# Kernel tuning notes

Measured on AMD Instinct MI355X. Metric: run time of the kernel, lower is better.

## Reference

```python
import jax, jax.numpy as jnp
import numpy as np

B, IN, H = 4096, 1024, 1024
G = 5  # i, f, o, c_hat, s gates

def setup_inputs() -> dict:
    key = jax.random.key(0)
    ks = jax.random.split(key, 24)
    s_in = 1.0 / np.sqrt(IN)
    s_h = 1.0 / np.sqrt(H)
    s_cat = 1.0 / np.sqrt(IN + H)
    inp = {
        'x': jax.random.normal(ks[0], (B, IN), jnp.float32),
        'h_prev': jax.random.normal(ks[1], (B, H), jnp.float32),
        'c_prev': jax.random.normal(ks[2], (B, H), jnp.float32),
        'ssg_state': jax.random.normal(ks[3], (B, H), jnp.float32),
        # stacked gate weights, torch Linear convention y = x @ W.T + b
        'Wx': jax.random.uniform(ks[4], (G, H, IN), jnp.float32, -s_in, s_in),
        'bWx': jax.random.uniform(ks[5], (G, H), jnp.float32, -s_in, s_in),
        'Ux': jax.random.uniform(ks[6], (G, H, H), jnp.float32, -s_h, s_h),
        'bUx': jax.random.uniform(ks[7], (G, H), jnp.float32, -s_h, s_h),
        # alpha MLP: Linear(IN+H -> H), ReLU, Linear(H -> 1), Sigmoid
        'a1_w': jax.random.uniform(ks[8], (H, IN + H), jnp.float32, -s_cat, s_cat),
        'a1_b': jax.random.uniform(ks[9], (H,), jnp.float32, -s_cat, s_cat),
        'a2_w': jax.random.uniform(ks[10], (1, H), jnp.float32, -s_h, s_h),
        'a2_b': jax.random.uniform(ks[11], (1,), jnp.float32, -s_h, s_h),
        'r1_w': jax.random.uniform(ks[12], (H, H), jnp.float32, -s_h, s_h),
        'r1_b': jax.random.uniform(ks[13], (H,), jnp.float32, -s_h, s_h),
        'r2_w': jax.random.uniform(ks[14], (H, H), jnp.float32, -s_h, s_h),
        'r2_b': jax.random.uniform(ks[15], (H,), jnp.float32, -s_h, s_h),
        'r3_w': jax.random.uniform(ks[16], (H, H), jnp.float32, -s_h, s_h),
        'r3_b': jax.random.uniform(ks[17], (H,), jnp.float32, -s_h, s_h),
        'ssg_w': jax.random.uniform(ks[18], (H, H), jnp.float32, -s_h, s_h),
        'ssg_b': jax.random.uniform(ks[19], (H,), jnp.float32, -s_h, s_h),
    }
    return inp


def reference(x, h_prev, c_prev, ssg_state, Wx, bWx, Ux, bUx,
              a1_w, a1_b, a2_w, a2_b, r1_w, r1_b, r2_w, r2_b, r3_w, r3_b,
              ssg_w, ssg_b):
    # all 5 gate pre-activations in two batched GEMMs: [G, B, H]
    g = (jnp.einsum('bi,ghi->gbh', x, Wx) + bWx[:, None, :]
         + jnp.einsum('bh,gkh->gbk', h_prev, Ux) + bUx[:, None, :])
    i_t = jax.nn.sigmoid(g[0])
    f_t = jax.nn.sigmoid(g[1])
    o_t = jax.nn.sigmoid(g[2])
    c_hat_t = jnp.tanh(g[3])
    s_t = jax.nn.sigmoid(g[4])  # computed as in original (unused when ssg_state given)

    combined = jnp.concatenate([x, h_prev], axis=-1)  # [B, IN+H]
    a_hidden = jax.nn.relu(combined @ a1_w.T + a1_b)
    alpha_t = jax.nn.sigmoid(a_hidden @ a2_w.T + a2_b)  # [B, 1]

    ssg_new = (ssg_state + h_prev) @ ssg_w.T + ssg_b  # ssg_state is not None branch

    c_t = f_t * c_prev + i_t * c_hat_t * s_t * alpha_t * ssg_new

    r = jax.nn.relu(h_prev @ r1_w.T + r1_b)
    r = jax.nn.relu(r @ r2_w.T + r2_b)
    residual = r @ r3_w.T + r3_b

    c_t = c_t + residual
    h_t = o_t * jnp.tanh(c_t)
    return (h_t, c_t, ssg_new)
```

## Files before the change

kernel.cpp:

```cpp
#include <hip/hip_runtime.h>
#include <hip/hip_bf16.h>

#define B_DIM 4096
#define H_DIM 1024
#define K1    2048
#define N1    6144

typedef __attribute__((ext_vector_type(8))) short bf16x8;
typedef __attribute__((ext_vector_type(4))) float f32x4;

__device__ __forceinline__ unsigned short f2bf(float f) {
  unsigned int x = __float_as_uint(f);
  x += 0x7fffu + ((x >> 16) & 1u);
  return (unsigned short)(x >> 16);
}
__device__ __forceinline__ float bf2f(unsigned short u) {
  return __uint_as_float(((unsigned int)u) << 16);
}
__device__ __forceinline__ float fast_sigmoid(float x) {
  return __builtin_amdgcn_rcpf(1.0f + __expf(-x));
}
__device__ __forceinline__ float fast_tanh(float x) {
  return 1.0f - 2.0f * __builtin_amdgcn_rcpf(1.0f + __expf(2.0f * x));
}
__device__ __forceinline__ void gload_lds16(const void* g, void* l) {
  __builtin_amdgcn_global_load_lds(
      (const __attribute__((address_space(1))) void*)g,
      (__attribute__((address_space(3))) void*)l, 16, 0, 0);
}

__device__ __forceinline__ int swz1k(int x) {
  return x ^ (((x >> 9) & 1) << 5);
}

__global__ __launch_bounds__(256) void prep_kernel(
    const float* __restrict__ x, const float* __restrict__ h,
    const float* __restrict__ ssg_state,
    const float* __restrict__ Wx, const float* __restrict__ Ux,
    const float* __restrict__ a1_w,
    const float* __restrict__ ssg_w, const float* __restrict__ r1_w,
    const float* __restrict__ r2_w, const float* __restrict__ r3_w,
    unsigned short* __restrict__ combined,
    unsigned short* __restrict__ ssg_in,
    unsigned short* __restrict__ W1,
    unsigned short* __restrict__ W2,
    unsigned short* __restrict__ W3,
    unsigned short* __restrict__ W4)
{
  const size_t NV0 = (size_t)B_DIM * K1 / 4;
  const size_t NV1 = (size_t)B_DIM * H_DIM / 4;
  const size_t NV3 = (size_t)N1 * K1 / 4;
  const size_t NV4 = (size_t)2048 * H_DIM / 4;
  const size_t NV5 = (size_t)H_DIM * H_DIM / 4;
  const size_t total = NV0 + NV1 + NV3 + NV4 + NV5 + NV5;
  const size_t stride = (size_t)gridDim.x * blockDim.x;

  for (size_t v = (size_t)blockIdx.x * blockDim.x + threadIdx.x; v < total; v += stride) {
    size_t idx = v;
    const float* src;
    unsigned short* dst;
    if (idx < NV0) {
      size_t e = idx * 4, b = e >> 11, k = e & 2047;
      src = (k < 1024) ? &x[(b << 10) + k] : &h[(b << 10) + (k - 1024)];
      dst = &combined[e];
    } else if ((idx -= NV0) < NV1) {
      size_t e = idx * 4;
      float4 a = *(const float4*)&ssg_state[e];
      float4 c = *(const float4*)&h[e];
      ushort4 o;
      o.x = f2bf(a.x + c.x); o.y = f2bf(a.y + c.y);
      o.z = f2bf(a.z + c.z); o.w = f2bf(a.w + c.w);
      *(ushort4*)&ssg_in[e] = o;
      continue;
    } else if ((idx -= NV1) < NV3) {
      size_t e = idx * 4, n = e >> 11, k = e & 2047;
      if (n < 5120) src = (k < 1024) ? &Wx[(n << 10) + k] : &Ux[(n << 10) + (k - 1024)];
      else          src = &a1_w[((n - 5120) << 11) + k];
      dst = &W1[e];
    } else if ((idx -= NV3) < NV4) {
      size_t e = idx * 4, n = e >> 10, k = e & 1023;
      src = (n < 1024) ? &ssg_w[(n << 10) + k] : &r1_w[((n - 1024) << 10) + k];
      dst = &W2[e];
    } else if ((idx -= NV4) < NV5) {
      size_t e = idx * 4; src = &r2_w[e]; dst = &W3[e];
    } else {
      idx -= NV5;
      size_t e = idx * 4; src = &r3_w[e]; dst = &W4[e];
    }
    float4 a = *(const float4*)src;
    ushort4 o;
    o.x = f2bf(a.x); o.y = f2bf(a.y); o.z = f2bf(a.z); o.w = f2bf(a.w);
    *(ushort4*)dst = o;
  }
}

template <int NT, int MODE>
__device__ __forceinline__ void gemm_body(
    unsigned short* lds, const int bid,
    const unsigned short* __restrict__ A0,
    const unsigned short* __restrict__ A1,
    const unsigned short* __restrict__ W,
    const float* __restrict__ b0, const float* __restrict__ b1,
    const float* __restrict__ b2,
    void* __restrict__ out0, void* __restrict__ out1)
{
  constexpr int KDIM = NT * 64;
  constexpr int NTN  = (MODE == 0) ? 48 : (MODE == 1 ? 16 : 8);
  constexpr int NWG  = 32 * NTN;

  const int tid  = threadIdx.x;
  const int wave = tid >> 6;
  const int lane = tid & 63;
  const int wm = wave >> 1;
  const int wn = wave & 1;

  const int swz = (bid & 7) * (NWG / 8) + (bid >> 3);
  const int tm = swz / NTN, tn = swz % NTN;
  const int tmB = tm * 128, tnB = tn * 128;

  const unsigned short* Abase = A0;
  int lda = (MODE == 0) ? K1 : 1024;
  if (MODE == 1 && tn >= 8) { Abase = A1; lda = 2048; }

  const int sidx = swz1k(lane * 16);
  const int r_l  = sidx >> 6;
  const int kel  = (sidx & 63) >> 1;
  const unsigned short* pA[2][2];
  const unsigned short* pB[2][2];
#pragma unroll
  for (int rg = 0; rg < 2; ++rg)
#pragma unroll
    for (int j = 0; j < 2; ++j) {
      const int rr = wave * 32 + rg * 16 + r_l;
      const int kk0 = j * 32 + kel;
      pA[rg][j] = Abase + (size_t)(tmB + rr) * lda + kk0;
      pB[rg][j] = W + (size_t)(tnB + rr) * KDIM + kk0;
    }

#define STAGE_A(tt) do { const int p_ = (tt) & 1;                                \
    _Pragma("unroll")                                                            \
    for (int rg = 0; rg < 2; ++rg)                                               \
      _Pragma("unroll")                                                          \
      for (int j = 0; j < 2; ++j)                                                \
        gload_lds16(pA[rg][j] + (size_t)(tt) * 64,                               \
                    &lds[p_ * 16384 + ((wave * 2 + rg) * 2 + j) * 512]);         \
  } while (0)
#define STAGE_B(tt) do { const int p_ = (tt) & 1;                                \
    _Pragma("unroll")                                                            \
    for (int rg = 0; rg < 2; ++rg)                                               \
      _Pragma("unroll")                                                          \
      for (int j = 0; j < 2; ++j)                                                \
        gload_lds16(pB[rg][j] + (size_t)(tt) * 64,                               \
                    &lds[p_ * 16384 + 8192 + ((wave * 2 + rg) * 2 + j) * 512]);  \
  } while (0)

  const int loc = swz1k((lane & 15) * 64 + (lane >> 4) * 16);

  f32x4 acc[4][4];
#pragma unroll
  for (int m = 0; m < 4; ++m)
#pragma unroll
    for (int n = 0; n < 4; ++n) acc[m][n] = (f32x4){0.f, 0.f, 0.f, 0.f};

  STAGE_A(0); STAGE_B(0);

#define MFMA16(aV, bV) do {                                                      \
    _Pragma("unroll")                                                            \
    for (int n = 0; n < 4; ++n) {                                                \
      _Pragma("unroll")                                                          \
      for (int m = 0; m < 4; ++m)                                                \
        acc[m][n] = __builtin_amdgcn_mfma_f32_16x16x32_bf16(                     \
            aV[m], bV[n], acc[m][n], 0, 0, 0);                                   \
    } } while (0)

  const char* lchar = (const char*)lds;
  for (int t = 0; t < NT; ++t) {
    asm volatile("s_waitcnt vmcnt(0)" ::: "memory");
    __builtin_amdgcn_s_barrier();

    const char* base = lchar + (t & 1) * 32768;
    const char* bA = base + wm * 8192 + loc;
    const char* bB = base + 16384 + wn * 8192 + loc;

    bf16x8 a0[4], a1[4], b0v[4], b1v[4];
#pragma unroll
    for (int n = 0; n < 4; ++n) b0v[n] = *(const bf16x8*)(bB + (2 * n + 0) * 1024);
#pragma unroll
    for (int m = 0; m < 4; ++m) a0[m] = *(const bf16x8*)(bA + (2 * m + 0) * 1024);
    if (t + 1 < NT) STAGE_A(t + 1);
#pragma unroll
    for (int n = 0; n < 4; ++n) b1v[n] = *(const bf16x8*)(bB + (2 * n + 1) * 1024);
#pragma unroll
    for (int m = 0; m < 4; ++m) a1[m] = *(const bf16x8*)(bA + (2 * m + 1) * 1024);
    if (t + 1 < NT) STAGE_B(t + 1);

    __builtin_amdgcn_s_setprio(1);
    MFMA16(a0, b0v);
    __builtin_amdgcn_s_setprio(0);
    __builtin_amdgcn_s_setprio(1);
    MFMA16(a1, b1v);
    __builtin_amdgcn_s_setprio(0);
  }
#undef MFMA16
#undef STAGE_A
#undef STAGE_B

  const int l15 = lane & 15, lq4 = (lane >> 4) << 2;
  const int rowg0 = tmB + wm * 64;

  if ((MODE == 1 && tn < 8) || MODE == 3) {
    const int col0 = tn * 128 + wn * 64;
#pragma unroll
    for (int fn = 0; fn < 4; ++fn) {
      const int col = col0 + fn * 16 + l15;
      const float bias = b0[col];
#pragma unroll
      for (int fm = 0; fm < 4; ++fm) {
        f32x4 v = acc[fm][fn];
#pragma unroll
        for (int j = 0; j < 4; ++j) {
          const int r = rowg0 + fm * 16 + lq4 + j;
          ((float*)out0)[(size_t)r * 1024 + col] = v[j] + bias;
        }
      }
    }
    return;
  }

  unsigned short* slab = &lds[wave * 1024];
  const int lr8 = lane >> 3, lc8 = lane & 7;
  bool isgate = false;
  int g = 0, colg0;
  unsigned short* outbase;
  if (MODE == 0) {
    isgate = (tn < 40);
    g = tn >> 3;
    colg0 = (isgate ? (tn & 7) : (tn - 40)) * 128 + wn * 64;
    outbase = isgate ? ((unsigned short*)out0 + (size_t)g * ((size_t)B_DIM * 1024))
                     : (unsigned short*)out1;
  } else if (MODE == 1) {
    colg0 = (tn - 8) * 128 + wn * 64;
    outbase = (unsigned short*)out1;
  } else {
    colg0 = tn * 128 + wn * 64;
    outbase = (unsigned short*)out1;
  }
  float biasv[4];
#pragma unroll
  for (int fn = 0; fn < 4; ++fn) {
    const int c = colg0 + fn * 16 + l15;
    if (MODE == 0) biasv[fn] = isgate ? (b0[g * 1024 + c] + b1[g * 1024 + c]) : b2[c];
    else           biasv[fn] = b1[c];
  }
  __builtin_amdgcn_s_barrier();
#pragma unroll
  for (int fm = 0; fm < 4; ++fm) {
#pragma unroll
    for (int fn = 0; fn < 4; ++fn) {
      f32x4 v = acc[fm][fn];
#pragma unroll
      for (int j = 0; j < 4; ++j) {
        const int row = lq4 + j;
        const float xv = v[j] + biasv[fn];
        float res;
        if (MODE == 0 && isgate) res = (g == 3) ? fast_tanh(xv) : fast_sigmoid(xv);
        else                     res = fmaxf(xv, 0.f);
        const int colb = ((fn * 16 + l15) * 2) ^ (((row >> 2) & 3) << 5);
        slab[(row * 128 + colb) >> 1] = f2bf(res);
      }
    }
    asm volatile("s_waitcnt lgkmcnt(0)" ::: "memory");
    __builtin_amdgcn_sched_barrier(0);
#pragma unroll
    for (int rd = 0; rd < 2; ++rd) {
      const int row = rd * 8 + lr8;
      const int cb = (lc8 * 16) ^ (((row >> 2) & 3) << 5);
      bf16x8 pk = *(const bf16x8*)((const char*)slab + row * 128 + cb);
      const size_t r = (size_t)(rowg0 + fm * 16 + row);
      *(bf16x8*)&outbase[r * 1024 + colg0 + lc8 * 8] = pk;
    }
    asm volatile("s_waitcnt lgkmcnt(0)" ::: "memory");
    __builtin_amdgcn_sched_barrier(0);
  }
}

__global__ __launch_bounds__(256, 2) void gemm_big(
    const unsigned short* __restrict__ combined,
    const unsigned short* __restrict__ ssg_in,
    const unsigned short* __restrict__ W1,
    const unsigned short* __restrict__ W2,
    const float* __restrict__ bWx, const float* __restrict__ bUx,
    const float* __restrict__ a1_b,
    const float* __restrict__ ssg_b, const float* __restrict__ r1_b,
    unsigned short* __restrict__ gates,
    unsigned short* __restrict__ a_hidden,
    float* __restrict__ ssg_out,
    unsigned short* __restrict__ r1)
{
  __shared__ unsigned short lds[32768];
  const int bid = blockIdx.x;
  if (bid < 1536) {
    gemm_body<32, 0>(lds, bid, combined, nullptr, W1,
                     bWx, bUx, a1_b, gates, a_hidden);
  } else {
    gemm_body<16, 1>(lds, bid - 1536, ssg_in, combined + 1024, W2,
                     ssg_b, r1_b, nullptr, ssg_out, r1);
  }
}

template <int MODE>
__global__ __launch_bounds__(256, 2) void gemm_small(
    const unsigned short* __restrict__ A,
    const unsigned short* __restrict__ W,
    const float* __restrict__ bias,
    void* __restrict__ out)
{
  __shared__ unsigned short lds[32768];
  if (MODE == 2) gemm_body<16, 2>(lds, blockIdx.x, A, nullptr, W,
                                  nullptr, bias, nullptr, nullptr, out);
  else           gemm_body<16, 3>(lds, blockIdx.x, A, nullptr, W,
                                  bias, nullptr, nullptr, out, nullptr);
}

__global__ __launch_bounds__(256) void final_fused(
    const unsigned short* __restrict__ gates,
    const float* __restrict__ c_prev,
    const unsigned short* __restrict__ a_hidden,
    const float* __restrict__ a2_w, const float* __restrict__ a2_b,
    const float* __restrict__ residual,
    const float* __restrict__ ssg_new,
    float* __restrict__ h_out, float* __restrict__ c_out)
{
  __shared__ float red[5];
  const int r = blockIdx.x;
  const int tid = threadIdx.x;
  const size_t BH = (size_t)B_DIM * H_DIM;

  {
    ushort4 u = *(const ushort4*)&a_hidden[(size_t)r * 1024 + tid * 4];
    float4 w = *(const float4*)&a2_w[tid * 4];
    float s = bf2f(u.x) * w.x + bf2f(u.y) * w.y + bf2f(u.z) * w.z + bf2f(u.w) * w.w;
#pragma unroll
    for (int off = 32; off; off >>= 1) s += __shfl_xor(s, off);
    if ((tid & 63) == 0) red[tid >> 6] = s;
  }
  __syncthreads();
  if (tid == 0)
    red[4] = fast_sigmoid(red[0] + red[1] + red[2] + red[3] + a2_b[0]);
  __syncthreads();
  const float al = red[4];

  const size_t e = (size_t)r * 1024 + tid * 4;
  ushort4 iu = *(const ushort4*)&gates[e];
  ushort4 fu = *(const ushort4*)&gates[BH + e];
  ushort4 ou = *(const ushort4*)&gates[2 * BH + e];
  ushort4 cu = *(const ushort4*)&gates[3 * BH + e];
  ushort4 su = *(const ushort4*)&gates[4 * BH + e];
  float4 cp = *(const float4*)&c_prev[e];
  float4 rs = *(const float4*)&residual[e];
  float4 sg = *(const float4*)&ssg_new[e];
  float4 ho, co;
  co.x = bf2f(fu.x) * cp.x + bf2f(iu.x) * bf2f(cu.x) * bf2f(su.x) * al * sg.x + rs.x;
  co.y = bf2f(fu.y) * cp.y + bf2f(iu.y) * bf2f(cu.y) * bf2f(su.y) * al * sg.y + rs.y;
  co.z = bf2f(fu.z) * cp.z + bf2f(iu.z) * bf2f(cu.z) * bf2f(su.z) * al * sg.z + rs.z;
  co.w = bf2f(fu.w) * cp.w + bf2f(iu.w) * bf2f(cu.w) * bf2f(su.w) * al * sg.w + rs.w;
  ho.x = bf2f(ou.x) * fast_tanh(co.x);
  ho.y = bf2f(ou.y) * fast_tanh(co.y);
  ho.z = bf2f(ou.z) * fast_tanh(co.z);
  ho.w = bf2f(ou.w) * fast_tanh(co.w);
  *(float4*)&h_out[e] = ho;
  *(float4*)&c_out[e] = co;
}

extern "C" void kernel_launch(void* const* d_in, const int* in_sizes, int n_in,
                              void* d_out, int out_size, void* d_ws, size_t ws_size,
                              hipStream_t stream)
{
  (void)in_sizes; (void)n_in; (void)out_size; (void)ws_size;
  const float* x         = (const float*)d_in[0];
  const float* h_prev    = (const float*)d_in[1];
  const float* c_prev    = (const float*)d_in[2];
  const float* ssg_state = (const float*)d_in[3];
  const float* Wx        = (const float*)d_in[4];
  const float* bWx       = (const float*)d_in[5];
  const float* Ux        = (const float*)d_in[6];
  const float* bUx       = (const float*)d_in[7];
  const float* a1_w      = (const float*)d_in[8];
  const float* a1_b      = (const float*)d_in[9];
  const float* a2_w      = (const float*)d_in[10];
  const float* a2_b      = (const float*)d_in[11];
  const float* r1_w      = (const float*)d_in[12];
  const float* r1_b      = (const float*)d_in[13];
  const float* r2_w      = (const float*)d_in[14];
  const float* r2_b      = (const float*)d_in[15];
  const float* r3_w      = (const float*)d_in[16];
  const float* r3_b      = (const float*)d_in[17];
  const float* ssg_w     = (const float*)d_in[18];
  const float* ssg_b     = (const float*)d_in[19];

  char* ws = (char*)d_ws;
  unsigned short* combined = (unsigned short*)(ws);
  unsigned short* ssg_in   = (unsigned short*)(ws + 16777216);
  unsigned short* W1       = (unsigned short*)(ws + 33554432);
  unsigned short* W2       = (unsigned short*)(ws + 58720256);
  unsigned short* W3       = (unsigned short*)(ws + 62914560);
  unsigned short* W4       = (unsigned short*)(ws + 65011712);
  unsigned short* gates    = (unsigned short*)(ws + 67108864);
  unsigned short* a_hidden = (unsigned short*)(ws + 109051904);
  unsigned short* r1       = (unsigned short*)(ws + 117456896);
  unsigned short* r2       = (unsigned short*)(ws + 125845504);
  float*          residual = (float*)(ws + 134234112);

  float* h_out   = (float*)d_out;
  float* c_out   = h_out + (size_t)B_DIM * H_DIM;
  float* ssg_out = c_out + (size_t)B_DIM * H_DIM;

  prep_kernel<<<4096, 256, 0, stream>>>(x, h_prev, ssg_state, Wx, Ux, a1_w,
                                        ssg_w, r1_w, r2_w, r3_w,
                                        combined, ssg_in, W1, W2, W3, W4);

  gemm_big<<<2048, 256, 0, stream>>>(
      combined, ssg_in, W1, W2, bWx, bUx, a1_b, ssg_b, r1_b,
      gates, a_hidden, ssg_out, r1);

  gemm_small<2><<<256, 256, 0, stream>>>(r1, W3, r2_b, r2);

  gemm_small<3><<<256, 256, 0, stream>>>(r2, W4, r3_b, residual);

  final_fused<<<B_DIM, 256, 0, stream>>>(
      gates, c_prev, a_hidden, a2_w, a2_b, residual, ssg_out, h_out, c_out);
}
```

Before: 224.0 us.

## Use 128x192 output tiles for the big gate GEMM to raise reuse

```diff
diff --git a/kernel.cpp b/kernel.cpp
--- a/kernel.cpp
+++ b/kernel.cpp
@@ -94,6 +94,169 @@
   }
 }
 
+__device__ __forceinline__ void body192(
+    unsigned short* lds, const int bid,
+    const unsigned short* __restrict__ A,
+    const unsigned short* __restrict__ W,
+    const float* __restrict__ bWx, const float* __restrict__ bUx,
+    const float* __restrict__ a1_b,
+    unsigned short* __restrict__ gates,
+    unsigned short* __restrict__ a_hidden)
+{
+  constexpr int NT  = 32;
+  constexpr int NTN = 32;
+  constexpr int NWG = 32 * NTN;
+
+  const int tid  = threadIdx.x;
+  const int wave = tid >> 6;
+  const int lane = tid & 63;
+  const int wm = wave >> 1;
+  const int wn = wave & 1;
+
+  const int swz = (bid & 7) * (NWG / 8) + (bid >> 3);
+  const int tm = swz / NTN, tn = swz % NTN;
+  const int tmB = tm * 128, tnB = tn * 192;
+
+  const int sidx = swz1k(lane * 16);
+  const int r_l  = sidx >> 6;
+  const int kel  = (sidx & 63) >> 1;
+  const unsigned short* pA[2][2];
+  const unsigned short* pB[3][2];
+#pragma unroll
+  for (int rg = 0; rg < 2; ++rg)
+#pragma unroll
+    for (int j = 0; j < 2; ++j)
+      pA[rg][j] = A + (size_t)(tmB + (wave * 2 + rg) * 16 + r_l) * K1 + j * 32 + kel;
+#pragma unroll
+  for (int rg = 0; rg < 3; ++rg)
+#pragma unroll
+    for (int j = 0; j < 2; ++j)
+      pB[rg][j] = W + (size_t)(tnB + (wave * 3 + rg) * 16 + r_l) * K1 + j * 32 + kel;
+
+#define STAGE_A(tt) do { const int p_ = (tt) & 1;                                \
+    _Pragma("unroll")                                                            \
+    for (int rg = 0; rg < 2; ++rg)                                               \
+      _Pragma("unroll")                                                          \
+      for (int j = 0; j < 2; ++j)                                                \
+        gload_lds16(pA[rg][j] + (size_t)(tt) * 64,                               \
+                    &lds[p_ * 20480 + ((wave * 2 + rg) * 2 + j) * 512]);         \
+  } while (0)
+#define STAGE_B(tt) do { const int p_ = (tt) & 1;                                \
+    _Pragma("unroll")                                                            \
+    for (int rg = 0; rg < 3; ++rg)                                               \
+      _Pragma("unroll")                                                          \
+      for (int j = 0; j < 2; ++j)                                                \
+        gload_lds16(pB[rg][j] + (size_t)(tt) * 64,                               \
+                    &lds[p_ * 20480 + 8192 + ((wave * 3 + rg) * 2 + j) * 512]);  \
+  } while (0)
+
+  const int loc = swz1k((lane & 15) * 64 + (lane >> 4) * 16);
+
+  f32x4 acc[4][6];
+#pragma unroll
+  for (int m = 0; m < 4; ++m)
+#pragma unroll
+    for (int n = 0; n < 6; ++n) acc[m][n] = (f32x4){0.f, 0.f, 0.f, 0.f};
+
+  STAGE_A(0); STAGE_B(0);
+
+#define MFMA24(aV, bV) do {                                                      \
+    _Pragma("unroll")                                                            \
+    for (int n = 0; n < 6; ++n) {                                                \
+      _Pragma("unroll")                                                          \
+      for (int m = 0; m < 4; ++m)                                                \
+        acc[m][n] = __builtin_amdgcn_mfma_f32_16x16x32_bf16(                     \
+            aV[m], bV[n], acc[m][n], 0, 0, 0);                                   \
+    } } while (0)
+
+  const char* lchar = (const char*)lds;
+  for (int t = 0; t < NT; ++t) {
+    asm volatile("s_waitcnt vmcnt(0)" ::: "memory");
+    __builtin_amdgcn_s_barrier();
+
+    const char* base = lchar + (t & 1) * 40960;
+    const char* bA = base + wm * 8192 + loc;
+    const char* bB = base + 16384 + wn * 12288 + loc;
+
+    bf16x8 a0[4], a1[4], b0[6], b1[6];
+#pragma unroll
+    for (int n = 0; n < 6; ++n) b0[n] = *(const bf16x8*)(bB + (2 * n + 0) * 1024);
+#pragma unroll
+    for (int m = 0; m < 4; ++m) a0[m] = *(const bf16x8*)(bA + (2 * m + 0) * 1024);
+    if (t + 1 < NT) STAGE_A(t + 1);
+#pragma unroll
+    for (int n = 0; n < 6; ++n) b1[n] = *(const bf16x8*)(bB + (2 * n + 1) * 1024);
+#pragma unroll
+    for (int m = 0; m < 4; ++m) a1[m] = *(const bf16x8*)(bA + (2 * m + 1) * 1024);
+    if (t + 1 < NT) STAGE_B(t + 1);
+
+    __builtin_amdgcn_s_setprio(1);
+    MFMA24(a0, b0);
+    __builtin_amdgcn_s_setprio(0);
+    __builtin_amdgcn_s_setprio(1);
+    MFMA24(a1, b1);
+    __builtin_amdgcn_s_setprio(0);
+  }
+#undef MFMA24
+#undef STAGE_A
+#undef STAGE_B
+
+  unsigned short* slab = &lds[wave * 1536];
+  const int l15 = lane & 15, lq4 = (lane >> 4) << 2;
+  const int colg0 = tnB + wn * 96;
+  const int rowg0 = tmB + wm * 64;
+  const size_t BH = (size_t)B_DIM * H_DIM;
+
+  float biasv[6];
+  int amode[6];
+#pragma unroll
+  for (int fn = 0; fn < 6; ++fn) {
+    const int c = colg0 + fn * 16 + l15;
+    if (c < 5120) {
+      biasv[fn] = bWx[c] + bUx[c];
+      amode[fn] = ((c >> 10) == 3) ? 1 : 0;
+    } else {
+      biasv[fn] = a1_b[c - 5120];
+      amode[fn] = 2;
+    }
+  }
+  __builtin_amdgcn_s_barrier();
+#pragma unroll
+  for (int fm = 0; fm < 4; ++fm) {
+#pragma unroll
+    for (int fn = 0; fn < 6; ++fn) {
+      f32x4 v = acc[fm][fn];
+#pragma unroll
+      for (int j = 0; j < 4; ++j) {
+        const int row = lq4 + j;
+        const float xv = v[j] + biasv[fn];
+        const float res = (amode[fn] == 1) ? fast_tanh(xv)
+                         : (amode[fn] == 0) ? fast_sigmoid(xv)
+                         : fmaxf(xv, 0.f);
+        const int byte = (row * 192 + (fn * 16 + l15) * 2) ^ (((row >> 2) & 1) << 5);
+        slab[byte >> 1] = f2bf(res);
+      }
+    }
+    asm volatile("s_waitcnt lgkmcnt(0)" ::: "memory");
+    __builtin_amdgcn_sched_barrier(0);
+#pragma unroll
+    for (int p = 0; p < 3; ++p) {
+      const int id = p * 64 + lane;
+      const int row = id / 12, cc = id - row * 12;
+      const int byte = (row * 192 + cc * 16) ^ (((row >> 2) & 1) << 5);
+      bf16x8 pk = *(const bf16x8*)((const char*)slab + byte);
+      const int col = colg0 + cc * 8;
+      const size_t r = (size_t)(rowg0 + fm * 16 + row);
+      unsigned short* dst;
+      if (col < 5120) dst = gates + (size_t)(col >> 10) * BH + r * 1024 + (col & 1023);
+      else            dst = a_hidden + r * 1024 + (col - 5120);
+      *(bf16x8*)dst = pk;
+    }
+    asm volatile("s_waitcnt lgkmcnt(0)" ::: "memory");
+    __builtin_amdgcn_sched_barrier(0);
+  }
+}
+
 template <int NT, int MODE>
 __device__ __forceinline__ void gemm_body(
     unsigned short* lds, const int bid,
@@ -101,11 +264,10 @@
     const unsigned short* __restrict__ A1,
     const unsigned short* __restrict__ W,
     const float* __restrict__ b0, const float* __restrict__ b1,
-    const float* __restrict__ b2,
     void* __restrict__ out0, void* __restrict__ out1)
 {
   constexpr int KDIM = NT * 64;
-  constexpr int NTN  = (MODE == 0) ? 48 : (MODE == 1 ? 16 : 8);
+  constexpr int NTN  = (MODE == 1) ? 16 : 8;
   constexpr int NWG  = 32 * NTN;
 
   const int tid  = threadIdx.x;
@@ -119,7 +281,7 @@
   const int tmB = tm * 128, tnB = tn * 128;
 
   const unsigned short* Abase = A0;
-  int lda = (MODE == 0) ? K1 : 1024;
+  int lda = 1024;
   if (MODE == 1 && tn >= 8) { Abase = A1; lda = 2048; }
 
   const int sidx = swz1k(lane * 16);
@@ -229,29 +391,13 @@
 
   unsigned short* slab = &lds[wave * 1024];
   const int lr8 = lane >> 3, lc8 = lane & 7;
-  bool isgate = false;
-  int g = 0, colg0;
-  unsigned short* outbase;
-  if (MODE == 0) {
-    isgate = (tn < 40);
-    g = tn >> 3;
-    colg0 = (isgate ? (tn & 7) : (tn - 40)) * 128 + wn * 64;
-    outbase = isgate ? ((unsigned short*)out0 + (size_t)g * ((size_t)B_DIM * 1024))
-                     : (unsigned short*)out1;
-  } else if (MODE == 1) {
-    colg0 = (tn - 8) * 128 + wn * 64;
-    outbase = (unsigned short*)out1;
-  } else {
-    colg0 = tn * 128 + wn * 64;
-    outbase = (unsigned short*)out1;
-  }
+  int colg0;
+  unsigned short* outbase = (unsigned short*)out1;
+  if (MODE == 1) colg0 = (tn - 8) * 128 + wn * 64;
+  else           colg0 = tn * 128 + wn * 64;
   float biasv[4];
 #pragma unroll
-  for (int fn = 0; fn < 4; ++fn) {
-    const int c = colg0 + fn * 16 + l15;
-    if (MODE == 0) biasv[fn] = isgate ? (b0[g * 1024 + c] + b1[g * 1024 + c]) : b2[c];
-    else           biasv[fn] = b1[c];
-  }
+  for (int fn = 0; fn < 4; ++fn) biasv[fn] = b1[colg0 + fn * 16 + l15];
   __builtin_amdgcn_s_barrier();
 #pragma unroll
   for (int fm = 0; fm < 4; ++fm) {
@@ -261,10 +407,7 @@
 #pragma unroll
       for (int j = 0; j < 4; ++j) {
         const int row = lq4 + j;
-        const float xv = v[j] + biasv[fn];
-        float res;
-        if (MODE == 0 && isgate) res = (g == 3) ? fast_tanh(xv) : fast_sigmoid(xv);
-        else                     res = fmaxf(xv, 0.f);
+        const float res = fmaxf(v[j] + biasv[fn], 0.f);
         const int colb = ((fn * 16 + l15) * 2) ^ (((row >> 2) & 3) << 5);
         slab[(row * 128 + colb) >> 1] = f2bf(res);
       }
@@ -297,14 +440,13 @@
     float* __restrict__ ssg_out,
     unsigned short* __restrict__ r1)
 {
-  __shared__ unsigned short lds[32768];
+  __shared__ unsigned short lds[40960];
   const int bid = blockIdx.x;
-  if (bid < 1536) {
-    gemm_body<32, 0>(lds, bid, combined, nullptr, W1,
-                     bWx, bUx, a1_b, gates, a_hidden);
+  if (bid < 1024) {
+    body192(lds, bid, combined, W1, bWx, bUx, a1_b, gates, a_hidden);
   } else {
-    gemm_body<16, 1>(lds, bid - 1536, ssg_in, combined + 1024, W2,
-                     ssg_b, r1_b, nullptr, ssg_out, r1);
+    gemm_body<16, 1>(lds, bid - 1024, ssg_in, combined + 1024, W2,
+                     ssg_b, r1_b, ssg_out, r1);
   }
 }
 
@@ -317,9 +459,9 @@
 {
   __shared__ unsigned short lds[32768];
   if (MODE == 2) gemm_body<16, 2>(lds, blockIdx.x, A, nullptr, W,
-                                  nullptr, bias, nullptr, nullptr, out);
+                                  nullptr, bias, nullptr, out);
   else           gemm_body<16, 3>(lds, blockIdx.x, A, nullptr, W,
-                                  bias, nullptr, nullptr, out, nullptr);
+                                  bias, nullptr, out, nullptr);
 }
 
 __global__ __launch_bounds__(256) void final_fused(
@@ -419,7 +561,7 @@
                                         ssg_w, r1_w, r2_w, r3_w,
                                         combined, ssg_in, W1, W2, W3, W4);
 
-  gemm_big<<<2048, 256, 0, stream>>>(
+  gemm_big<<<1536, 256, 0, stream>>>(
       combined, ssg_in, W1, W2, bWx, bUx, a1_b, ssg_b, r1_b,
       gates, a_hidden, ssg_out, r1);
 
```

New measurement: 219.7 us. About the same (-1.9%).
